# Kernel tuning notes

Measured on AMD Instinct MI355X. Metric: run time of the kernel, lower is better.

The kernel has to match this reference:

```python
import jax, jax.numpy as jnp
import numpy as np

KS = (3, 4, 3)          # kernel_size per pseudo-coordinate dim
OPEN = (1, 0, 1)        # is_open_spline per dim
K = 36                  # prod(KS)
STRIDES = (12, 3, 1)    # mixed-radix strides for flat kernel index
DIM = 3
S = 8                   # 2**DIM basis products per edge (degree-1 B-spline)


def spline_basis(pseudo):
    """pseudo: [E,3] in [0,1]. Returns basis weights B [E,8] and flat kernel idx WI [E,8]."""
    ws, idxs = [], []
    for d in range(DIM):
        k = KS[d]
        u = pseudo[:, d]
        if OPEN[d]:
            v = u * (k - 1)
            fl = jnp.floor(v)
            f = v - fl
            i0 = jnp.clip(fl, 0, k - 1)
            i1 = jnp.clip(i0 + 1, 0, k - 1)
        else:
            v = u * k
            fl = jnp.floor(v)
            f = v - fl
            i0 = jnp.mod(fl, k)
            i1 = jnp.mod(fl + 1, k)
        ws.append(jnp.stack([1.0 - f, f], axis=1))            # [E,2]
        idxs.append(jnp.stack([i0, i1], axis=1).astype(jnp.int32))
    Bs, WIs = [], []
    for s in range(S):
        bits = [(s >> d) & 1 for d in range(DIM)]
        b = ws[0][:, bits[0]] * ws[1][:, bits[1]] * ws[2][:, bits[2]]
        wi = (idxs[0][:, bits[0]] * STRIDES[0]
              + idxs[1][:, bits[1]] * STRIDES[1]
              + idxs[2][:, bits[2]] * STRIDES[2])
        Bs.append(b)
        WIs.append(wi)
    return jnp.stack(Bs, axis=1), jnp.stack(WIs, axis=1)


def spline_conv(x, src, dst, B, WI, deg_inv, W, root, bias):
    """Spline conv: scatter basis-weighted source feats into [N*K,Fin] buckets, then one GEMM."""
    N, Fin = x.shape
    Fout = W.shape[2]
    x_j = x[src]                                   # [E,Fin] gather
    A = jnp.zeros((N * K, Fin), dtype=x.dtype)
    for s in range(S):                             # fixed small loop over 8 basis terms
        A = A + jax.ops.segment_sum(B[:, s:s + 1] * x_j, dst * K + WI[:, s], num_segments=N * K)
    out = A.reshape(N, K * Fin) @ W.reshape(K * Fin, Fout)
    return out * deg_inv[:, None] + x @ root + bias


def setup_inputs() -> dict:
    N, E = 20000, 320000
    key = jax.random.key(0)
    ks = jax.random.split(key, 16)
    inp = {
        "x": jax.random.normal(ks[0], (N, 1), dtype=jnp.float32),
        "pseudo": jax.random.uniform(ks[1], (E, 3), dtype=jnp.float32),
        "edge_index": jax.random.randint(ks[2], (2, E), 0, N, dtype=jnp.int32),
        "W1": jax.random.normal(ks[3], (K, 1, 32), dtype=jnp.float32) * 0.1,
        "root1": jax.random.normal(ks[4], (1, 32), dtype=jnp.float32) * 0.1,
        "b1": jnp.zeros((32,), dtype=jnp.float32),
        "W2": jax.random.normal(ks[5], (K, 32, 64), dtype=jnp.float32) * 0.05,
        "root2": jax.random.normal(ks[6], (32, 64), dtype=jnp.float32) * 0.05,
        "b2": jnp.zeros((64,), dtype=jnp.float32),
        "W3": jax.random.normal(ks[7], (K, 64, 128), dtype=jnp.float32) * 0.03,
        "root3": jax.random.normal(ks[8], (64, 128), dtype=jnp.float32) * 0.03,
        "b3": jnp.zeros((128,), dtype=jnp.float32),
        "lw1": jax.random.normal(ks[9], (128, 256), dtype=jnp.float32) * 0.05,
        "lb1": jnp.zeros((256,), dtype=jnp.float32),
        "lw2": jax.random.normal(ks[10], (256, 6890), dtype=jnp.float32) * 0.05,
        "lb2": jnp.zeros((6890,), dtype=jnp.float32),
    }
    return inp


def reference(x, pseudo, edge_index, W1, root1, b1, W2, root2, b2, W3, root3, b3, lw1, lb1, lw2, lb2):
    N = x.shape[0]
    src, dst = edge_index[0], edge_index[1]
    B, WI = spline_basis(pseudo)
    deg = jax.ops.segment_sum(jnp.ones_like(dst, dtype=x.dtype), dst, num_segments=N)
    deg_inv = 1.0 / jnp.maximum(deg, 1.0)          # mean aggregation
    h = jax.nn.relu(spline_conv(x, src, dst, B, WI, deg_inv, W1, root1, b1))
    h = jax.nn.relu(spline_conv(h, src, dst, B, WI, deg_inv, W2, root2, b2))
    h = jax.nn.relu(spline_conv(h, src, dst, B, WI, deg_inv, W3, root3, b3))
    h = jax.nn.relu(h @ lw1 + lb1)
    # dropout is identity in eval mode
    logits = h @ lw2 + lb2
    return jax.nn.log_softmax(logits, axis=-1)
```

## Files before the change

### kernel.cpp

```cpp
#include <hip/hip_runtime.h>
#include <math.h>


#define KCONV 36

typedef __attribute__((ext_vector_type(4))) float f32x4;
typedef __attribute__((ext_vector_type(4))) int int4v;
typedef __attribute__((ext_vector_type(8))) short short8;

__device__ __forceinline__ unsigned bf16_rne(float x) {
    unsigned u = __builtin_bit_cast(unsigned, x);
    return (u + 0x7FFFu + ((u >> 16) & 1u)) >> 16;
}
__device__ __forceinline__ float bf16_f(unsigned h) {
    return __builtin_bit_cast(float, h << 16);
}

__global__ void basis_kernel(const float* __restrict__ pseudo,
                             float* __restrict__ B, int* __restrict__ WI, int E) {
    int e = blockIdx.x * blockDim.x + threadIdx.x;
    if (e >= E) return;
    float f[3]; int i0[3], i1[3];
    {
        float v = pseudo[e * 3 + 0] * 2.0f;
        float fl = floorf(v); f[0] = v - fl;
        float c0 = fminf(fmaxf(fl, 0.f), 2.f);
        i0[0] = (int)c0; i1[0] = (int)fminf(c0 + 1.f, 2.f);
    }
    {
        float v = pseudo[e * 3 + 1] * 4.0f;
        float fl = floorf(v); f[1] = v - fl;
        i0[1] = (int)fmodf(fl, 4.f); i1[1] = (int)fmodf(fl + 1.f, 4.f);
    }
    {
        float v = pseudo[e * 3 + 2] * 2.0f;
        float fl = floorf(v); f[2] = v - fl;
        float c0 = fminf(fmaxf(fl, 0.f), 2.f);
        i0[2] = (int)c0; i1[2] = (int)fminf(c0 + 1.f, 2.f);
    }
#pragma unroll
    for (int s = 0; s < 8; ++s) {
        int b0 = s & 1, b1 = (s >> 1) & 1, b2 = (s >> 2) & 1;
        float w = (b0 ? f[0] : 1.f - f[0]) * (b1 ? f[1] : 1.f - f[1]) * (b2 ? f[2] : 1.f - f[2]);
        int wi = (b0 ? i1[0] : i0[0]) * 12 + (b1 ? i1[1] : i0[1]) * 3 + (b2 ? i1[2] : i0[2]);
        B[e * 8 + s] = w;
        WI[e * 8 + s] = wi;
    }
}

__global__ void hist_kernel(const int* __restrict__ dst, int* __restrict__ cnt, int E) {
    int e = blockIdx.x * blockDim.x + threadIdx.x;
    if (e < E) atomicAdd(&cnt[dst[e]], 1);
}

__global__ __launch_bounds__(1024) void scan_kernel(
    const int* __restrict__ cnt, int* __restrict__ ptr, int* __restrict__ cur,
    float* __restrict__ deginv, int N) {
    __shared__ int sdata[1024];
    __shared__ int carry;
    int tid = threadIdx.x;
    if (tid == 0) carry = 0;
    __syncthreads();
    for (int base = 0; base < N; base += 1024) {
        int i = base + tid;
        int v = (i < N) ? cnt[i] : 0;
        sdata[tid] = v;
        __syncthreads();
        for (int off = 1; off < 1024; off <<= 1) {
            int t = (tid >= off) ? sdata[tid - off] : 0;
            __syncthreads();
            sdata[tid] += t;
            __syncthreads();
        }
        int excl = carry + sdata[tid] - v;
        if (i < N) {
            ptr[i] = excl;
            cur[i] = excl;
            deginv[i] = 1.0f / fmaxf((float)v, 1.0f);
        }
        __syncthreads();
        if (tid == 0) carry += sdata[1023];
        __syncthreads();
    }
    if (tid == 0) ptr[N] = carry;
}

__global__ void fill_kernel(const int* __restrict__ dst, int* __restrict__ cur,
                            int* __restrict__ eid, int E) {
    int e = blockIdx.x * blockDim.x + threadIdx.x;
    if (e < E) {
        int p = atomicAdd(&cur[dst[e]], 1);
        eid[p] = e;
    }
}

__global__ void scaleB_kernel(float* __restrict__ B, const int* __restrict__ dst,
                              const float* __restrict__ deginv, int E) {
    int idx = blockIdx.x * blockDim.x + threadIdx.x;
    if (idx < E * 8) B[idx] *= deginv[dst[idx >> 3]];
}

__global__ __launch_bounds__(256) void gather1_kernel(
    const float* __restrict__ x, const int* __restrict__ src,
    const float* __restrict__ B, const int* __restrict__ WI,
    const int* __restrict__ ptr, const int* __restrict__ eid,
    float* __restrict__ A, int N) {
    __shared__ float accs[256 * 37];
    int t = threadIdx.x;
    int node = blockIdx.x * 256 + t;
    float* a = &accs[t * 37];
#pragma unroll
    for (int w = 0; w < KCONV; ++w) a[w] = 0.f;
    if (node >= N) return;
    int i0 = ptr[node], i1 = ptr[node + 1];
    for (int i = i0; i < i1; ++i) {
        int e = eid[i];
        float xv = x[src[e]];
        const float* Bp = B + (size_t)e * 8;
        const int* Wp = WI + (size_t)e * 8;
        f32x4 b0 = *(const f32x4*)Bp, b1 = *(const f32x4*)(Bp + 4);
        int4v w0 = *(const int4v*)Wp, w1 = *(const int4v*)(Wp + 4);
#pragma unroll
        for (int s = 0; s < 4; ++s) a[w0[s]] += b0[s] * xv;
#pragma unroll
        for (int s = 0; s < 4; ++s) a[w1[s]] += b1[s] * xv;
    }
#pragma unroll
    for (int w = 0; w < KCONV; ++w) A[(size_t)node * KCONV + w] = a[w];
}

template <int F>
__global__ __launch_bounds__(256) void gatherF_kernel(
    const float* __restrict__ h, const int* __restrict__ src,
    const float* __restrict__ B, const int* __restrict__ WI,
    const int* __restrict__ ptr, const int* __restrict__ eid,
    float* __restrict__ A, int N) {
    constexpr int NPB = 256 / F;
    __shared__ float accs[NPB * KCONV * F];
    int t = threadIdx.x;
    int f = t & (F - 1);
    int g = t / F;
    int node = blockIdx.x * NPB + g;
    float* a = &accs[(size_t)g * KCONV * F + f];
#pragma unroll
    for (int w = 0; w < KCONV; ++w) a[w * F] = 0.f;
    if (node >= N) return;
    int i0 = ptr[node], i1 = ptr[node + 1];
    for (int i = i0; i < i1; ++i) {
        int e = eid[i];
        float xv = h[(size_t)src[e] * F + f];
        const float* Bp = B + (size_t)e * 8;
        const int* Wp = WI + (size_t)e * 8;
        f32x4 b0 = *(const f32x4*)Bp, b1 = *(const f32x4*)(Bp + 4);
        int4v w0 = *(const int4v*)Wp, w1 = *(const int4v*)(Wp + 4);
#pragma unroll
        for (int s = 0; s < 4; ++s) a[w0[s] * F] += b0[s] * xv;
#pragma unroll
        for (int s = 0; s < 4; ++s) a[w1[s] * F] += b1[s] * xv;
    }
#pragma unroll
    for (int w = 0; w < KCONV; ++w)
        A[((size_t)node * KCONV + w) * F + f] = a[w * F];
}

__global__ void packB_kernel(const float* __restrict__ W, int K1,
                             const float* __restrict__ R, int K2,
                             int N, int Np,
                             unsigned short* __restrict__ Bhi,
                             unsigned short* __restrict__ Blo) {
    int ks = blockIdx.x, nf = blockIdx.y;
    int lane = threadIdx.x;
    int n = nf * 16 + (lane & 15);
    int kg = lane >> 4;
    size_t dst = (((size_t)ks * (Np >> 4) + nf) * 64 + lane) * 8;
#pragma unroll
    for (int j = 0; j < 8; ++j) {
        int k = ks * 32 + kg * 8 + j;
        float v = 0.f;
        if (n < N) v = (k < K1) ? W[(size_t)k * N + n] : R[(size_t)(k - K1) * N + n];
        unsigned h = bf16_rne(v);
        unsigned l = bf16_rne(v - bf16_f(h));
        Bhi[dst + j] = (unsigned short)h;
        Blo[dst + j] = (unsigned short)l;
    }
}

__global__ __launch_bounds__(256) void gemm_bf3_kernel(
    const float* __restrict__ A, int K1,
    const float* __restrict__ X, int K2,
    const unsigned short* __restrict__ Bhi, const unsigned short* __restrict__ Blo,
    const float* __restrict__ bias, float* __restrict__ C,
    int M, int N, int Np, int relu) {
    __shared__ unsigned short sAh[4096], sAl[4096], sBh[4096], sBl[4096];
    const int t = threadIdx.x, lane = t & 63, wave = t >> 6;
    const int wr = wave >> 1, wc = wave & 1;
    const int m0 = blockIdx.y * 128, n0 = blockIdx.x * 128;
    const int Kp = K1 + K2, nks = Kp >> 5;
    const int npf = Np >> 4;
    const int rowA = lane & 15, kg = lane >> 4;

    f32x4 acc[4][4];
#pragma unroll
    for (int i = 0; i < 4; ++i)
#pragma unroll
        for (int j = 0; j < 4; ++j) acc[i][j] = (f32x4){0.f, 0.f, 0.f, 0.f};

    for (int ks = 0; ks < nks; ++ks) {
        __syncthreads();
#pragma unroll
        for (int r = 0; r < 2; ++r) {
            int fm = wave + r * 4;
            int row = m0 + fm * 16 + rowA;
            int kk = (ks << 5) + (kg << 3);
            f32x4 p0 = {0.f, 0.f, 0.f, 0.f}, p1 = {0.f, 0.f, 0.f, 0.f};
            if (row < M) {
                const float* sp = (kk < K1) ? (A + (size_t)row * K1 + kk)
                                            : (X + (size_t)row * K2 + (kk - K1));
                p0 = *(const f32x4*)sp;
                p1 = *(const f32x4*)(sp + 4);
            }
            short8 hv, lv;
#pragma unroll
            for (int j = 0; j < 8; ++j) {
                float a = (j < 4) ? p0[j] : p1[j - 4];
                unsigned h = bf16_rne(a);
                unsigned l = bf16_rne(a - bf16_f(h));
                hv[j] = (short)h;
                lv[j] = (short)l;
            }
            int doff = (fm * 64 + lane) * 8;
            *(short8*)(&sAh[doff]) = hv;
            *(short8*)(&sAl[doff]) = lv;
        }
#pragma unroll
        for (int r = 0; r < 2; ++r) {
            int fn = wave + r * 4;
            size_t soff = (((size_t)ks * npf + (n0 >> 4) + fn) * 64 + lane) * 8;
            short8 hb = *(const short8*)(Bhi + soff);
            short8 lb = *(const short8*)(Blo + soff);
            int doff = (fn * 64 + lane) * 8;
            *(short8*)(&sBh[doff]) = hb;
            *(short8*)(&sBl[doff]) = lb;
        }
        __syncthreads();

        short8 ah[4], al[4], bh[4], bl[4];
#pragma unroll
        for (int i = 0; i < 4; ++i) {
            int off = ((wr * 4 + i) * 64 + lane) * 8;
            ah[i] = *(const short8*)(&sAh[off]);
            al[i] = *(const short8*)(&sAl[off]);
        }
#pragma unroll
        for (int j = 0; j < 4; ++j) {
            int off = ((wc * 4 + j) * 64 + lane) * 8;
            bh[j] = *(const short8*)(&sBh[off]);
            bl[j] = *(const short8*)(&sBl[off]);
        }
#pragma unroll
        for (int i = 0; i < 4; ++i)
#pragma unroll
            for (int j = 0; j < 4; ++j) {
                acc[i][j] = __builtin_amdgcn_mfma_f32_16x16x32_bf16(ah[i], bh[j], acc[i][j], 0, 0, 0);
                acc[i][j] = __builtin_amdgcn_mfma_f32_16x16x32_bf16(ah[i], bl[j], acc[i][j], 0, 0, 0);
                acc[i][j] = __builtin_amdgcn_mfma_f32_16x16x32_bf16(al[i], bh[j], acc[i][j], 0, 0, 0);
            }
    }

#pragma unroll
    for (int i = 0; i < 4; ++i) {
        int rbase = m0 + wr * 64 + i * 16 + (lane >> 4) * 4;
#pragma unroll
        for (int j = 0; j < 4; ++j) {
            int col = n0 + wc * 64 + j * 16 + (lane & 15);
            if (col >= N) continue;
            float bz = bias ? bias[col] : 0.f;
#pragma unroll
            for (int r = 0; r < 4; ++r) {
                int row = rbase + r;
                if (row < M) {
                    float v = acc[i][j][r] + bz;
                    if (relu) v = fmaxf(v, 0.f);
                    C[(size_t)row * N + col] = v;
                }
            }
        }
    }
}

__global__ __launch_bounds__(256) void gemm_kernel(
    const float* __restrict__ A, const float* __restrict__ W, int K1,
    const float* __restrict__ X, const float* __restrict__ R, int K2,
    const float* __restrict__ bias, float* __restrict__ C,
    int M, int N, int relu) {
    __shared__ float As[16][65];
    __shared__ float Bs[16][65];
    int t = threadIdx.x;
    int tx = t & 15, ty = t >> 4;
    int m0 = blockIdx.y * 64, n0 = blockIdx.x * 64;
    float acc[4][4] = {};
    const float* Ap = A;
    const float* Wp = W;
    int K = K1;
    for (int pass = 0; pass < 2; ++pass) {
        if (pass == 1) {
            if (K2 == 0 || X == nullptr) break;
            Ap = X; Wp = R; K = K2;
        }
        for (int k0 = 0; k0 < K; k0 += 16) {
#pragma unroll
            for (int l = 0; l < 4; ++l) {
                int idx = t + l * 256;
                int i = idx >> 4, kk = idx & 15;
                int m = m0 + i, k = k0 + kk;
                As[kk][i] = (m < M && k < K) ? Ap[(long)m * K + k] : 0.f;
            }
#pragma unroll
            for (int l = 0; l < 4; ++l) {
                int idx = t + l * 256;
                int kk = idx >> 6, j = idx & 63;
                int k = k0 + kk, n = n0 + j;
                Bs[kk][j] = (k < K && n < N) ? Wp[(long)k * N + n] : 0.f;
            }
            __syncthreads();
#pragma unroll
            for (int kk = 0; kk < 16; ++kk) {
                float a[4], b[4];
#pragma unroll
                for (int i = 0; i < 4; ++i) a[i] = As[kk][ty + 16 * i];
#pragma unroll
                for (int j = 0; j < 4; ++j) b[j] = Bs[kk][tx + 16 * j];
#pragma unroll
                for (int i = 0; i < 4; ++i)
#pragma unroll
                    for (int j = 0; j < 4; ++j) acc[i][j] += a[i] * b[j];
            }
            __syncthreads();
        }
    }
#pragma unroll
    for (int i = 0; i < 4; ++i) {
        int m = m0 + ty + 16 * i;
        if (m >= M) continue;
#pragma unroll
        for (int j = 0; j < 4; ++j) {
            int n = n0 + tx + 16 * j;
            if (n >= N) continue;
            float v = acc[i][j];
            if (bias) v += bias[n];
            if (relu) v = fmaxf(v, 0.f);
            C[(long)m * N + n] = v;
        }
    }
}

__global__ __launch_bounds__(256) void logsoftmax_kernel(float* __restrict__ out, int C) {
    int row = blockIdx.x;
    float* p = out + (long)row * C;
    __shared__ float red[256];
    float mx = -INFINITY;
    for (int c = threadIdx.x; c < C; c += 256) mx = fmaxf(mx, p[c]);
    red[threadIdx.x] = mx;
    __syncthreads();
    for (int s = 128; s > 0; s >>= 1) {
        if (threadIdx.x < s) red[threadIdx.x] = fmaxf(red[threadIdx.x], red[threadIdx.x + s]);
        __syncthreads();
    }
    mx = red[0];
    __syncthreads();
    float sum = 0.f;
    for (int c = threadIdx.x; c < C; c += 256) sum += expf(p[c] - mx);
    red[threadIdx.x] = sum;
    __syncthreads();
    for (int s = 128; s > 0; s >>= 1) {
        if (threadIdx.x < s) red[threadIdx.x] += red[threadIdx.x + s];
        __syncthreads();
    }
    float lse = logf(red[0]) + mx;
    for (int c = threadIdx.x; c < C; c += 256) p[c] = p[c] - lse;
}

extern "C" void kernel_launch(void* const* d_in, const int* in_sizes, int n_in,
                              void* d_out, int out_size, void* d_ws, size_t ws_size,
                              hipStream_t stream) {
    const float* x      = (const float*)d_in[0];
    const float* pseudo = (const float*)d_in[1];
    const int*   ei     = (const int*)d_in[2];
    const float* W1     = (const float*)d_in[3];
    const float* root1  = (const float*)d_in[4];
    const float* b1     = (const float*)d_in[5];
    const float* W2     = (const float*)d_in[6];
    const float* root2  = (const float*)d_in[7];
    const float* b2     = (const float*)d_in[8];
    const float* W3     = (const float*)d_in[9];
    const float* root3  = (const float*)d_in[10];
    const float* b3     = (const float*)d_in[11];
    const float* lw1    = (const float*)d_in[12];
    const float* lb1    = (const float*)d_in[13];
    const float* lw2    = (const float*)d_in[14];
    const float* lb2    = (const float*)d_in[15];

    const int N = in_sizes[0];
    const int E = in_sizes[1] / 3;
    const int Cout = 6890;
    const int* src = ei;
    const int* dst = ei + E;

    float* ws = (float*)d_ws;
    size_t off = 0;
    float* B      = ws + off; off += (size_t)E * 8;
    int*   WI     = (int*)(ws + off); off += (size_t)E * 8;
    float* deginv = ws + off; off += N;
    int*   cnt    = (int*)(ws + off); off += N;
    int*   ptr    = (int*)(ws + off); off += N + 1;
    int*   cur    = (int*)(ws + off); off += N;
    int*   eid    = (int*)(ws + off); off += E;
    float* h1  = ws + off; off += (size_t)N * 32;
    float* h2  = ws + off; off += (size_t)N * 64;
    float* h3  = ws + off; off += (size_t)N * 128;
    float* h4  = ws + off; off += (size_t)N * 256;
    float* A   = ws + off; off += (size_t)N * KCONV * 64;
    unsigned short* pk = (unsigned short*)(ws + off);
    const size_t n2 = (size_t)1184 * 128, n3 = (size_t)2368 * 128;
    const size_t nl1 = (size_t)128 * 256, nl2 = (size_t)256 * 6912;
    unsigned short* B2h = pk;        pk += n2;
    unsigned short* B2l = pk;        pk += n2;
    unsigned short* B3h = pk;        pk += n3;
    unsigned short* B3l = pk;        pk += n3;
    unsigned short* L1h = pk;        pk += nl1;
    unsigned short* L1l = pk;        pk += nl1;
    unsigned short* L2h = pk;        pk += nl2;
    unsigned short* L2l = pk;        pk += nl2;
    float* out = (float*)d_out;

    packB_kernel<<<dim3(37, 8), 64, 0, stream>>>(W2, 1152, root2, 32, 64, 128, B2h, B2l);
    packB_kernel<<<dim3(74, 8), 64, 0, stream>>>(W3, 2304, root3, 64, 128, 128, B3h, B3l);
    packB_kernel<<<dim3(4, 16), 64, 0, stream>>>(lw1, 128, nullptr, 0, 256, 256, L1h, L1l);
    packB_kernel<<<dim3(8, 432), 64, 0, stream>>>(lw2, 256, nullptr, 0, Cout, 6912, L2h, L2l);

    basis_kernel<<<(E + 255) / 256, 256, 0, stream>>>(pseudo, B, WI, E);
    hipMemsetAsync(cnt, 0, (size_t)N * sizeof(int), stream);
    hist_kernel<<<(E + 255) / 256, 256, 0, stream>>>(dst, cnt, E);
    scan_kernel<<<1, 1024, 0, stream>>>(cnt, ptr, cur, deginv, N);
    scaleB_kernel<<<(E * 8 + 255) / 256, 256, 0, stream>>>(B, dst, deginv, E);
    fill_kernel<<<(E + 255) / 256, 256, 0, stream>>>(dst, cur, eid, E);

    const int mt = (N + 127) / 128;

    gather1_kernel<<<(N + 255) / 256, 256, 0, stream>>>(x, src, B, WI, ptr, eid, A, N);
    {
        dim3 g(1, (N + 63) / 64);
        gemm_kernel<<<g, 256, 0, stream>>>(A, W1, KCONV, x, root1, 1, b1, h1, N, 32, 1);
    }

    gatherF_kernel<32><<<(N + 7) / 8, 256, 0, stream>>>(h1, src, B, WI, ptr, eid, A, N);
    gemm_bf3_kernel<<<dim3(1, mt), 256, 0, stream>>>(A, 1152, h1, 32, B2h, B2l, b2, h2, N, 64, 128, 1);

    gatherF_kernel<64><<<(N + 3) / 4, 256, 0, stream>>>(h2, src, B, WI, ptr, eid, A, N);
    gemm_bf3_kernel<<<dim3(1, mt), 256, 0, stream>>>(A, 2304, h2, 64, B3h, B3l, b3, h3, N, 128, 128, 1);

    gemm_bf3_kernel<<<dim3(2, mt), 256, 0, stream>>>(h3, 128, nullptr, 0, L1h, L1l, lb1, h4, N, 256, 256, 1);
    gemm_bf3_kernel<<<dim3(54, mt), 256, 0, stream>>>(h4, 256, nullptr, 0, L2h, L2l, lb2, out, N, Cout, 6912, 0);
    logsoftmax_kernel<<<N, 256, 0, stream>>>(out, Cout);
}
```

Measured before the change: 1.917 ms.

## Fuse log-softmax partials into final GEMM and prepack hidden activations as bf16 fragments

```diff
diff --git a/kernel.cpp b/kernel.cpp
--- a/kernel.cpp
+++ b/kernel.cpp
@@ -7,6 +7,13 @@
 typedef __attribute__((ext_vector_type(4))) float f32x4;
 typedef __attribute__((ext_vector_type(4))) int int4v;
 typedef __attribute__((ext_vector_type(8))) short short8;
+
+typedef const unsigned __attribute__((address_space(1)))* gasp;
+typedef unsigned __attribute__((address_space(3)))* lasp;
+
+__device__ __forceinline__ void gld16(const void* g, unsigned short* l) {
+    __builtin_amdgcn_global_load_lds((gasp)g, (lasp)l, 16, 0, 0);
+}
 
 __device__ __forceinline__ unsigned bf16_rne(float x) {
     unsigned u = __builtin_bit_cast(unsigned, x);
@@ -56,33 +63,43 @@
 __global__ __launch_bounds__(1024) void scan_kernel(
     const int* __restrict__ cnt, int* __restrict__ ptr, int* __restrict__ cur,
     float* __restrict__ deginv, int N) {
-    __shared__ int sdata[1024];
-    __shared__ int carry;
-    int tid = threadIdx.x;
-    if (tid == 0) carry = 0;
+    __shared__ int wsum[16];
+    __shared__ int carry_s;
+    int tid = threadIdx.x, lane = tid & 63, wid = tid >> 6;
+    if (tid == 0) carry_s = 0;
     __syncthreads();
     for (int base = 0; base < N; base += 1024) {
         int i = base + tid;
         int v = (i < N) ? cnt[i] : 0;
-        sdata[tid] = v;
-        __syncthreads();
-        for (int off = 1; off < 1024; off <<= 1) {
-            int t = (tid >= off) ? sdata[tid - off] : 0;
-            __syncthreads();
-            sdata[tid] += t;
-            __syncthreads();
-        }
-        int excl = carry + sdata[tid] - v;
+        int x = v;
+        for (int off = 1; off < 64; off <<= 1) {
+            int t = __shfl_up(x, off, 64);
+            if (lane >= off) x += t;
+        }
+        if (lane == 63) wsum[wid] = x;
+        int carry = carry_s;
+        __syncthreads();
+        if (wid == 0) {
+            int w = (lane < 16) ? wsum[lane] : 0;
+            for (int off = 1; off < 16; off <<= 1) {
+                int t = __shfl_up(w, off, 64);
+                if (lane >= off) w += t;
+            }
+            if (lane < 16) wsum[lane] = w;
+        }
+        __syncthreads();
+        int wexcl = (wid == 0) ? 0 : wsum[wid - 1];
+        int excl = carry + wexcl + x - v;
         if (i < N) {
             ptr[i] = excl;
             cur[i] = excl;
             deginv[i] = 1.0f / fmaxf((float)v, 1.0f);
         }
         __syncthreads();
-        if (tid == 0) carry += sdata[1023];
-        __syncthreads();
-    }
-    if (tid == 0) ptr[N] = carry;
+        if (tid == 0) carry_s = carry + wsum[15];
+        __syncthreads();
+    }
+    if (threadIdx.x == 0) ptr[N] = carry_s;
 }
 
 __global__ void fill_kernel(const int* __restrict__ dst, int* __restrict__ cur,
@@ -285,6 +302,239 @@
                 }
             }
         }
+    }
+}
+
+__global__ __launch_bounds__(256) void gemm_bf3p_kernel(
+    const float* __restrict__ A, int K1,
+    const unsigned short* __restrict__ Bhi, const unsigned short* __restrict__ Blo,
+    const float* __restrict__ bias,
+    unsigned short* __restrict__ Ph, unsigned short* __restrict__ Pl,
+    int nkso, int M, int N, int Np) {
+    __shared__ unsigned short sAh[4096], sAl[4096], sBh[4096], sBl[4096];
+    const int t = threadIdx.x, lane = t & 63, wave = t >> 6;
+    const int wr = wave >> 1, wc = wave & 1;
+    const int m0 = blockIdx.y * 128, n0 = blockIdx.x * 128;
+    const int nks = K1 >> 5;
+    const int npf = Np >> 4;
+    const int rowA = lane & 15, kg = lane >> 4;
+    const int l15 = lane & 15;
+
+    f32x4 acc[4][4];
+#pragma unroll
+    for (int i = 0; i < 4; ++i)
+#pragma unroll
+        for (int j = 0; j < 4; ++j) acc[i][j] = (f32x4){0.f, 0.f, 0.f, 0.f};
+
+    for (int ks = 0; ks < nks; ++ks) {
+        __syncthreads();
+#pragma unroll
+        for (int r = 0; r < 2; ++r) {
+            int fm = wave + r * 4;
+            int row = m0 + fm * 16 + rowA;
+            int kk = (ks << 5) + (kg << 3);
+            f32x4 p0 = {0.f, 0.f, 0.f, 0.f}, p1 = {0.f, 0.f, 0.f, 0.f};
+            if (row < M) {
+                const float* sp = A + (size_t)row * K1 + kk;
+                p0 = *(const f32x4*)sp;
+                p1 = *(const f32x4*)(sp + 4);
+            }
+            short8 hv, lv;
+#pragma unroll
+            for (int j = 0; j < 8; ++j) {
+                float a = (j < 4) ? p0[j] : p1[j - 4];
+                unsigned h = bf16_rne(a);
+                unsigned l = bf16_rne(a - bf16_f(h));
+                hv[j] = (short)h;
+                lv[j] = (short)l;
+            }
+            int doff = (fm * 64 + lane) * 8;
+            *(short8*)(&sAh[doff]) = hv;
+            *(short8*)(&sAl[doff]) = lv;
+        }
+#pragma unroll
+        for (int r = 0; r < 2; ++r) {
+            int fn = wave + r * 4;
+            size_t soff = (((size_t)ks * npf + (n0 >> 4) + fn) * 64 + lane) * 8;
+            short8 hb = *(const short8*)(Bhi + soff);
+            short8 lb = *(const short8*)(Blo + soff);
+            int doff = (fn * 64 + lane) * 8;
+            *(short8*)(&sBh[doff]) = hb;
+            *(short8*)(&sBl[doff]) = lb;
+        }
+        __syncthreads();
+
+        short8 ah[4], al[4], bh[4], bl[4];
+#pragma unroll
+        for (int i = 0; i < 4; ++i) {
+            int off = ((wr * 4 + i) * 64 + lane) * 8;
+            ah[i] = *(const short8*)(&sAh[off]);
+            al[i] = *(const short8*)(&sAl[off]);
+        }
+#pragma unroll
+        for (int j = 0; j < 4; ++j) {
+            int off = ((wc * 4 + j) * 64 + lane) * 8;
+            bh[j] = *(const short8*)(&sBh[off]);
+            bl[j] = *(const short8*)(&sBl[off]);
+        }
+#pragma unroll
+        for (int i = 0; i < 4; ++i)
+#pragma unroll
+            for (int j = 0; j < 4; ++j) {
+                acc[i][j] = __builtin_amdgcn_mfma_f32_16x16x32_bf16(ah[i], bh[j], acc[i][j], 0, 0, 0);
+                acc[i][j] = __builtin_amdgcn_mfma_f32_16x16x32_bf16(ah[i], bl[j], acc[i][j], 0, 0, 0);
+                acc[i][j] = __builtin_amdgcn_mfma_f32_16x16x32_bf16(al[i], bh[j], acc[i][j], 0, 0, 0);
+            }
+    }
+
+#pragma unroll
+    for (int i = 0; i < 4; ++i) {
+        int rf = (m0 >> 4) + wr * 4 + i;
+#pragma unroll
+        for (int j = 0; j < 4; ++j) {
+            int col = n0 + wc * 64 + j * 16 + l15;
+            float bz = bias[col];
+            int ks = col >> 5;
+            int lanep = (kg * 4) + ((col >> 3) & 3) * 16;
+            int jj = col & 7;
+#pragma unroll
+            for (int r = 0; r < 4; ++r) {
+                int row = m0 + wr * 64 + i * 16 + kg * 4 + r;
+                if (row >= M) continue;
+                float v = fmaxf(acc[i][j][r] + bz, 0.f);
+                unsigned h = bf16_rne(v);
+                unsigned lo = bf16_rne(v - bf16_f(h));
+                size_t di = (((size_t)rf * nkso + ks) * 64 + lanep + r) * 8 + jj;
+                Ph[di] = (unsigned short)h;
+                Pl[di] = (unsigned short)lo;
+            }
+        }
+    }
+}
+
+__global__ __launch_bounds__(256) void gemm_lse_kernel(
+    const unsigned short* __restrict__ Ah, const unsigned short* __restrict__ Al,
+    const unsigned short* __restrict__ Bh, const unsigned short* __restrict__ Bl,
+    const float* __restrict__ bias, float* __restrict__ C,
+    float* __restrict__ pm, float* __restrict__ pl,
+    int M, int N, int nks, int npf, int nct, int nrt, int Mpad) {
+    __shared__ unsigned short sAh[4096], sAl[4096], sBh[4096], sBl[4096];
+    const int t = threadIdx.x, lane = t & 63, wave = t >> 6;
+    const int wr = wave >> 1, wc = wave & 1;
+    const int kg = lane >> 4, l15 = lane & 15;
+
+    int bid = blockIdx.x;
+    int nwg = nct * nrt;
+    int xcd = bid & 7, loc = bid >> 3;
+    int q = nwg >> 3, r8 = nwg & 7;
+    int wg = (xcd < r8 ? xcd * (q + 1) : r8 * (q + 1) + (xcd - r8) * q) + loc;
+    int rt = wg / nct, ct = wg - rt * nct;
+    const int m0 = rt * 128, n0 = ct * 128;
+
+    f32x4 acc[4][4];
+#pragma unroll
+    for (int i = 0; i < 4; ++i)
+#pragma unroll
+        for (int j = 0; j < 4; ++j) acc[i][j] = (f32x4){0.f, 0.f, 0.f, 0.f};
+
+    for (int ks = 0; ks < nks; ++ks) {
+        __syncthreads();
+#pragma unroll
+        for (int r2 = 0; r2 < 2; ++r2) {
+            int fm = wave + r2 * 4;
+            size_t afo = (((size_t)(rt * 8 + fm) * nks + ks) * 1024) + (size_t)lane * 16;
+            size_t bfo = (((size_t)ks * npf + ct * 8 + fm) * 1024) + (size_t)lane * 16;
+            gld16((const char*)Ah + afo, &sAh[fm * 512]);
+            gld16((const char*)Al + afo, &sAl[fm * 512]);
+            gld16((const char*)Bh + bfo, &sBh[fm * 512]);
+            gld16((const char*)Bl + bfo, &sBl[fm * 512]);
+        }
+        __syncthreads();
+
+        short8 ah[4], al[4], bh[4], bl[4];
+#pragma unroll
+        for (int i = 0; i < 4; ++i) {
+            int off = ((wr * 4 + i) * 64 + lane) * 8;
+            ah[i] = *(const short8*)(&sAh[off]);
+            al[i] = *(const short8*)(&sAl[off]);
+        }
+#pragma unroll
+        for (int j = 0; j < 4; ++j) {
+            int off = ((wc * 4 + j) * 64 + lane) * 8;
+            bh[j] = *(const short8*)(&sBh[off]);
+            bl[j] = *(const short8*)(&sBl[off]);
+        }
+#pragma unroll
+        for (int i = 0; i < 4; ++i)
+#pragma unroll
+            for (int j = 0; j < 4; ++j) {
+                acc[i][j] = __builtin_amdgcn_mfma_f32_16x16x32_bf16(ah[i], bh[j], acc[i][j], 0, 0, 0);
+                acc[i][j] = __builtin_amdgcn_mfma_f32_16x16x32_bf16(ah[i], bl[j], acc[i][j], 0, 0, 0);
+                acc[i][j] = __builtin_amdgcn_mfma_f32_16x16x32_bf16(al[i], bh[j], acc[i][j], 0, 0, 0);
+            }
+    }
+
+#pragma unroll
+    for (int i = 0; i < 4; ++i) {
+#pragma unroll
+        for (int r = 0; r < 4; ++r) {
+            int row = m0 + wr * 64 + i * 16 + kg * 4 + r;
+            float v[4];
+            float rmax = -INFINITY;
+#pragma unroll
+            for (int j = 0; j < 4; ++j) {
+                int col = n0 + wc * 64 + j * 16 + l15;
+                if (col < N) {
+                    float tv = acc[i][j][r] + bias[col];
+                    v[j] = tv;
+                    if (row < M) C[(size_t)row * N + col] = tv;
+                    rmax = fmaxf(rmax, tv);
+                } else {
+                    v[j] = -INFINITY;
+                }
+            }
+#pragma unroll
+            for (int o = 1; o < 16; o <<= 1) rmax = fmaxf(rmax, __shfl_xor(rmax, o, 64));
+            float s = 0.f;
+#pragma unroll
+            for (int j = 0; j < 4; ++j)
+                if (v[j] != -INFINITY) s += __expf(v[j] - rmax);
+#pragma unroll
+            for (int o = 1; o < 16; o <<= 1) s += __shfl_xor(s, o, 64);
+            if (l15 == 0 && row < M) {
+                int pidx = ct * 2 + wc;
+                pm[(size_t)pidx * Mpad + row] = rmax;
+                pl[(size_t)pidx * Mpad + row] = s;
+            }
+        }
+    }
+}
+
+__global__ void lse_kernel(const float* __restrict__ pm, const float* __restrict__ pl,
+                           float* __restrict__ lse, int M, int Mpad, int np) {
+    int rix = blockIdx.x * 256 + threadIdx.x;
+    if (rix >= M) return;
+    float m = -INFINITY, l = 0.f;
+    for (int p = 0; p < np; ++p) {
+        float mp = pm[(size_t)p * Mpad + rix];
+        float lp = pl[(size_t)p * Mpad + rix];
+        float mn = fmaxf(m, mp);
+        l = l * expf(m - mn) + lp * expf(mp - mn);
+        m = mn;
+    }
+    lse[rix] = m + logf(l);
+}
+
+__global__ __launch_bounds__(256) void sub_kernel(float* __restrict__ out,
+                                                  const float* __restrict__ lse, int C) {
+    int row = blockIdx.x;
+    float s = lse[row];
+    float2* p = (float2*)(out + (size_t)row * C);
+    int n2 = C >> 1;
+    for (int c = threadIdx.x; c < n2; c += 256) {
+        float2 v = p[c];
+        v.x -= s; v.y -= s;
+        p[c] = v;
     }
 }
 
@@ -352,32 +602,6 @@
             C[(long)m * N + n] = v;
         }
     }
-}
-
-__global__ __launch_bounds__(256) void logsoftmax_kernel(float* __restrict__ out, int C) {
-    int row = blockIdx.x;
-    float* p = out + (long)row * C;
-    __shared__ float red[256];
-    float mx = -INFINITY;
-    for (int c = threadIdx.x; c < C; c += 256) mx = fmaxf(mx, p[c]);
-    red[threadIdx.x] = mx;
-    __syncthreads();
-    for (int s = 128; s > 0; s >>= 1) {
-        if (threadIdx.x < s) red[threadIdx.x] = fmaxf(red[threadIdx.x], red[threadIdx.x + s]);
-        __syncthreads();
-    }
-    mx = red[0];
-    __syncthreads();
-    float sum = 0.f;
-    for (int c = threadIdx.x; c < C; c += 256) sum += expf(p[c] - mx);
-    red[threadIdx.x] = sum;
-    __syncthreads();
-    for (int s = 128; s > 0; s >>= 1) {
-        if (threadIdx.x < s) red[threadIdx.x] += red[threadIdx.x + s];
-        __syncthreads();
-    }
-    float lse = logf(red[0]) + mx;
-    for (int c = threadIdx.x; c < C; c += 256) p[c] = p[c] - lse;
 }
 
 extern "C" void kernel_launch(void* const* d_in, const int* in_sizes, int n_in,
@@ -406,6 +630,11 @@
     const int* src = ei;
     const int* dst = ei + E;
 
+    const int mt = (N + 127) / 128;
+    const int Mpad = mt * 128;
+    const int nct = 54;
+    const int nrf = Mpad / 16;
+
     float* ws = (float*)d_ws;
     size_t off = 0;
     float* B      = ws + off; off += (size_t)E * 8;
@@ -418,11 +647,11 @@
     float* h1  = ws + off; off += (size_t)N * 32;
     float* h2  = ws + off; off += (size_t)N * 64;
     float* h3  = ws + off; off += (size_t)N * 128;
-    float* h4  = ws + off; off += (size_t)N * 256;
     float* A   = ws + off; off += (size_t)N * KCONV * 64;
     unsigned short* pk = (unsigned short*)(ws + off);
-    const size_t n2 = (size_t)1184 * 128, n3 = (size_t)2368 * 128;
-    const size_t nl1 = (size_t)128 * 256, nl2 = (size_t)256 * 6912;
+    const size_t n2 = (size_t)37 * 8 * 512, n3 = (size_t)74 * 8 * 512;
+    const size_t nl1 = (size_t)4 * 16 * 512, nl2 = (size_t)8 * 432 * 512;
+    const size_t na4 = (size_t)nrf * 8 * 512;
     unsigned short* B2h = pk;        pk += n2;
     unsigned short* B2l = pk;        pk += n2;
     unsigned short* B3h = pk;        pk += n3;
@@ -431,6 +660,11 @@
     unsigned short* L1l = pk;        pk += nl1;
     unsigned short* L2h = pk;        pk += nl2;
     unsigned short* L2l = pk;        pk += nl2;
+    unsigned short* A4h = pk;        pk += na4;
+    unsigned short* A4l = pk;        pk += na4;
+    float* pmb = (float*)pk;
+    float* plb = pmb + (size_t)nct * 2 * Mpad;
+    float* lseb = plb + (size_t)nct * 2 * Mpad;
     float* out = (float*)d_out;
 
     packB_kernel<<<dim3(37, 8), 64, 0, stream>>>(W2, 1152, root2, 32, 64, 128, B2h, B2l);
@@ -445,8 +679,6 @@
     scaleB_kernel<<<(E * 8 + 255) / 256, 256, 0, stream>>>(B, dst, deginv, E);
     fill_kernel<<<(E + 255) / 256, 256, 0, stream>>>(dst, cur, eid, E);
 
-    const int mt = (N + 127) / 128;
-
     gather1_kernel<<<(N + 255) / 256, 256, 0, stream>>>(x, src, B, WI, ptr, eid, A, N);
     {
         dim3 g(1, (N + 63) / 64);
@@ -459,7 +691,10 @@
     gatherF_kernel<64><<<(N + 3) / 4, 256, 0, stream>>>(h2, src, B, WI, ptr, eid, A, N);
     gemm_bf3_kernel<<<dim3(1, mt), 256, 0, stream>>>(A, 2304, h2, 64, B3h, B3l, b3, h3, N, 128, 128, 1);
 
-    gemm_bf3_kernel<<<dim3(2, mt), 256, 0, stream>>>(h3, 128, nullptr, 0, L1h, L1l, lb1, h4, N, 256, 256, 1);
-    gemm_bf3_kernel<<<dim3(54, mt), 256, 0, stream>>>(h4, 256, nullptr, 0, L2h, L2l, lb2, out, N, Cout, 6912, 0);
-    logsoftmax_kernel<<<N, 256, 0, stream>>>(out, Cout);
-}
+    gemm_bf3p_kernel<<<dim3(2, mt), 256, 0, stream>>>(h3, 128, L1h, L1l, lb1, A4h, A4l, 8, N, 256, 256);
+
+    gemm_lse_kernel<<<nct * mt, 256, 0, stream>>>(A4h, A4l, L2h, L2l, lb2, out,
+                                                  pmb, plb, N, Cout, 8, 432, nct, mt, Mpad);
+    lse_kernel<<<(N + 255) / 256, 256, 0, stream>>>(pmb, plb, lseb, N, Mpad, nct * 2);
+    sub_kernel<<<N, 256, 0, stream>>>(out, lseb, Cout);
+}
```

Measured after the change: 1.709 ms. -10.8%, faster.
